# Optimization experiments

Measured on AMD Instinct MI355X. Metric: run time of the kernel, lower is better.

Reference implementation:

```python
import jax, jax.numpy as jnp
import numpy as np

N, D, H, E = 50000, 128, 128, 800000


def setup_inputs() -> dict:
    key = jax.random.key(0)
    ks = jax.random.split(key, 12)
    p = lambda k, shape: jax.random.normal(k, shape, dtype=jnp.float32) * 0.02
    z = lambda n: jnp.zeros((n,), jnp.float32)
    return {
        "x1": jax.random.normal(ks[0], (N, D), dtype=jnp.float32),
        "edge_index1": jax.random.randint(ks[1], (2, E), 0, N, dtype=jnp.int32),
        "x2": jax.random.normal(ks[2], (N, D), dtype=jnp.float32),
        "edge_index2": jax.random.randint(ks[3], (2, E), 0, N, dtype=jnp.int32),
        "enc_w1": p(ks[4], (D, H)), "enc_b1": z(H),
        "enc_w2": p(ks[5], (H, H)), "enc_b2": z(H),
        "conv1_w": p(ks[6], (H, H)), "conv1_b": z(H),
        "conv2_w": p(ks[7], (H, H)), "conv2_b": z(H),
        "sim_w1": p(ks[8], (4 * H, H)), "sim_b1": z(H),
        "sim_w2": p(ks[9], (H, 1)), "sim_b2": z(1),
    }


def reference(x1, edge_index1, x2, edge_index2,
              enc_w1, enc_b1, enc_w2, enc_b2,
              conv1_w, conv1_b, conv2_w, conv2_b,
              sim_w1, sim_b1, sim_w2, sim_b2):
    def gcn(x, ei, W, b):
        row, col = ei[0], ei[1]            # [E], [E]
        h = x @ W + b                      # [N, H]
        n = x.shape[0]
        deg = jax.ops.segment_sum(jnp.ones(row.shape[0], h.dtype), row, num_segments=n)
        dis = jnp.where(deg > 0, deg ** -0.5, 0.0)   # deg^-0.5, inf -> 0
        norm = dis[row] * dis[col]         # [E]
        msg = h[col] * norm[:, None]       # gather + per-edge scale, [E, H]
        return jax.ops.segment_sum(msg, row, num_segments=n)  # scatter-add

    def embed(x, ei):
        h = jax.nn.relu(x @ enc_w1 + enc_b1) @ enc_w2 + enc_b2  # encoder MLP
        h = jax.nn.relu(gcn(h, ei, conv1_w, conv1_b))
        h = jax.nn.relu(gcn(h, ei, conv2_w, conv2_b))
        return h.mean(axis=0)              # mean pooling -> [H]

    g1 = embed(x1, edge_index1)
    g2 = embed(x2, edge_index2)
    c = jnp.concatenate([g1, g2, jnp.abs(g1 - g2), g1 * g2], axis=-1)  # [4H]
    return jax.nn.relu(c @ sim_w1 + sim_b1) @ sim_w2 + sim_b2          # [1]
```

## Files before the change

### kernel.cpp

```cpp
#include <hip/hip_runtime.h>

#define HD 128

typedef _Float16 f16x8 __attribute__((ext_vector_type(8)));
typedef _Float16 f16x2 __attribute__((ext_vector_type(2)));
typedef float f32x4 __attribute__((ext_vector_type(4)));

__device__ __forceinline__ void role_map(int bi, int S, int k, int& role, int& rid) {
  int q = bi / k, rem = bi - q * k;
  if (rem == 0 && q < S) { role = 1; rid = q; }
  else { role = 0; int na = q + (rem ? 1 : 0); if (na > S) na = S; rid = bi - na; }
}

__global__ void k_wcvt(const float* __restrict__ w0, const float* __restrict__ w1,
                       const float* __restrict__ w2, const float* __restrict__ w3,
                       _Float16* __restrict__ Wf) {
  int m = blockIdx.x >> 3;
  const float* Wg = (m == 0) ? w0 : (m == 1) ? w1 : (m == 2) ? w2 : w3;
  int idx0 = (blockIdx.x & 7) * 2048 + threadIdx.x * 8;
  float4 u0 = *(const float4*)(Wg + idx0);
  float4 u1 = *(const float4*)(Wg + idx0 + 4);
  int k = idx0 >> 7, n0 = idx0 & 127;
  int kc = k >> 5, q2 = (k >> 3) & 3, j = k & 7;
  _Float16* dst = Wf + (size_t)m * 16384;
  float vv[8] = {u0.x, u0.y, u0.z, u0.w, u1.x, u1.y, u1.z, u1.w};
  #pragma unroll
  for (int d = 0; d < 8; ++d) {
    int n = n0 + d;
    dst[(size_t)(((n >> 4) * 4 + kc) * 64 + 16 * q2 + (n & 15)) * 8 + j] = (_Float16)vv[d];
  }
}

__device__ __forceinline__ void deg_core(int rid, int degB,
    const int* __restrict__ ei0, const int* __restrict__ ei1, int E, int N,
    int* __restrict__ deg2, unsigned short* __restrict__ slot) {
  int g = (rid >= degB);
  int cb = rid - g * degB;
  const int* rows = g ? ei1 : ei0;
  int* deg = deg2 + g * N;
  unsigned short* sl = slot + (size_t)g * E;
  int base = (cb * 256 + threadIdx.x) * 4;
  if (base + 3 < E) {
    int4 r = *(const int4*)(rows + base);
    union { unsigned short us[4]; uint2 v; } s;
    s.us[0] = (unsigned short)atomicAdd(&deg[r.x], 1);
    s.us[1] = (unsigned short)atomicAdd(&deg[r.y], 1);
    s.us[2] = (unsigned short)atomicAdd(&deg[r.z], 1);
    s.us[3] = (unsigned short)atomicAdd(&deg[r.w], 1);
    *(uint2*)(sl + base) = s.v;
  } else {
    for (int e = base; e < E; ++e)
      sl[e] = (unsigned short)atomicAdd(&deg[rows[e]], 1);
  }
}

__device__ __forceinline__ void fill_core(int rid, int fillB,
    const int* __restrict__ ei0, const int* __restrict__ ei1, int E, int N,
    const int* __restrict__ offs, const int* __restrict__ partials,
    const unsigned short* __restrict__ slot, unsigned short* __restrict__ csr_col) {
  int g = (rid >= fillB);
  int cb = rid - g * fillB;
  const int* eg = (g ? ei1 : ei0);
  const int* ob = offs + g * N;
  const unsigned short* sl = slot + (size_t)g * E;
  int gN = g * N;
  int base = (cb * 256 + threadIdx.x) * 4;
  if (base + 3 < E) {
    int4 r = *(const int4*)(eg + base);
    int4 c = *(const int4*)(eg + E + base);
    uint2 sv = *(const uint2*)(sl + base);
    csr_col[ob[r.x] + partials[(gN + r.x) >> 8] + (sv.x & 0xffff)] = (unsigned short)c.x;
    csr_col[ob[r.y] + partials[(gN + r.y) >> 8] + (sv.x >> 16)]    = (unsigned short)c.y;
    csr_col[ob[r.z] + partials[(gN + r.z) >> 8] + (sv.y & 0xffff)] = (unsigned short)c.z;
    csr_col[ob[r.w] + partials[(gN + r.w) >> 8] + (sv.y >> 16)]    = (unsigned short)c.w;
  } else {
    for (int e = base; e < E; ++e)
      csr_col[ob[eg[e]] + partials[(gN + eg[e]) >> 8] + sl[e]] = (unsigned short)eg[E + e];
  }
}

__device__ __forceinline__ void gemm_core(_Float16* lds, int bi,
    const _Float16* __restrict__ Ab, const _Float16* __restrict__ Wf,
    const float* __restrict__ bias, const float* __restrict__ scale,
    _Float16* __restrict__ C, int Ntot) {
  const int tid = threadIdx.x;
  #pragma unroll
  for (int i = 0; i < 8; ++i)
    *(float4*)&lds[tid * 8 + i * 2048] = *(const float4*)&Wf[tid * 8 + i * 2048];
  __syncthreads();

  const int lane = tid & 63, wave = tid >> 6;
  const int n16 = lane & 15, q = lane >> 4;
  const int rowbase = bi * 128 + wave * 32;

  int arow[2];
  #pragma unroll
  for (int t = 0; t < 2; ++t) {
    int r = rowbase + 16 * t + n16;
    arow[t] = (r < Ntot) ? r : (Ntot - 1);
  }
  f32x4 acc[2][8];
  #pragma unroll
  for (int t = 0; t < 2; ++t)
    #pragma unroll
    for (int nt = 0; nt < 8; ++nt) acc[t][nt] = (f32x4){0.f, 0.f, 0.f, 0.f};

  #pragma unroll
  for (int kc = 0; kc < 4; ++kc) {
    f16x8 a[2];
    #pragma unroll
    for (int t = 0; t < 2; ++t)
      a[t] = *(const f16x8*)(Ab + (size_t)arow[t] * HD + kc * 32 + q * 8);
    #pragma unroll
    for (int nt = 0; nt < 8; ++nt) {
      f16x8 b = *(const f16x8*)&lds[(size_t)((nt * 4 + kc) * 64 + lane) * 8];
      #pragma unroll
      for (int t = 0; t < 2; ++t)
        acc[t][nt] = __builtin_amdgcn_mfma_f32_16x16x32_f16(a[t], b, acc[t][nt], 0, 0, 0);
    }
  }
  float bv[8];
  #pragma unroll
  for (int nt = 0; nt < 8; ++nt) bv[nt] = bias[nt * 16 + n16];
  #pragma unroll
  for (int t = 0; t < 2; ++t) {
    #pragma unroll
    for (int r = 0; r < 4; ++r) {
      int row = rowbase + 16 * t + 4 * q + r;
      if (row < Ntot) {
        float s = scale[row];
        #pragma unroll
        for (int nt = 0; nt < 8; ++nt) {
          float v = (acc[t][nt][r] + bv[nt]) * s;
          C[(size_t)row * HD + nt * 16 + n16] = (_Float16)v;
        }
      }
    }
  }
}

__device__ __forceinline__ void chain_core(_Float16* act, int bi,
    const float* __restrict__ x0, const float* __restrict__ x1,
    const _Float16* __restrict__ Wf0, const _Float16* __restrict__ Wf1,
    const float* __restrict__ b1, const float* __restrict__ b2,
    _Float16* __restrict__ H, int N, int Ntot) {
  const int tid = threadIdx.x;
  const int lane = tid & 63, wave = tid >> 6;
  const int n16 = lane & 15, q = lane >> 4;
  const int rowbase = bi * 128 + wave * 32;
  _Float16* wact = act + wave * 4352;

  int arow[2];
  #pragma unroll
  for (int t = 0; t < 2; ++t) {
    int r = rowbase + 16 * t + n16;
    arow[t] = (r < Ntot) ? r : (Ntot - 1);
  }
  f32x4 acc[2][8];
  #pragma unroll
  for (int t = 0; t < 2; ++t)
    #pragma unroll
    for (int nt = 0; nt < 8; ++nt) acc[t][nt] = (f32x4){0.f, 0.f, 0.f, 0.f};

  #pragma unroll
  for (int kc = 0; kc < 4; ++kc) {
    f16x8 a[2];
    #pragma unroll
    for (int t = 0; t < 2; ++t) {
      int r = arow[t];
      const float* src = (r < N) ? (x0 + (size_t)r * HD) : (x1 + (size_t)(r - N) * HD);
      float4 u0 = *(const float4*)(src + kc * 32 + q * 8);
      float4 u1 = *(const float4*)(src + kc * 32 + q * 8 + 4);
      union { _Float16 h[8]; f16x8 v; } tmp;
      tmp.h[0] = (_Float16)u0.x; tmp.h[1] = (_Float16)u0.y;
      tmp.h[2] = (_Float16)u0.z; tmp.h[3] = (_Float16)u0.w;
      tmp.h[4] = (_Float16)u1.x; tmp.h[5] = (_Float16)u1.y;
      tmp.h[6] = (_Float16)u1.z; tmp.h[7] = (_Float16)u1.w;
      a[t] = tmp.v;
    }
    #pragma unroll
    for (int nt = 0; nt < 8; ++nt) {
      f16x8 b = *(const f16x8*)&Wf0[(size_t)((nt * 4 + kc) * 64 + lane) * 8];
      #pragma unroll
      for (int t = 0; t < 2; ++t)
        acc[t][nt] = __builtin_amdgcn_mfma_f32_16x16x32_f16(a[t], b, acc[t][nt], 0, 0, 0);
    }
  }
  {
    float bv[8];
    #pragma unroll
    for (int nt = 0; nt < 8; ++nt) bv[nt] = b1[nt * 16 + n16];
    #pragma unroll
    for (int t = 0; t < 2; ++t)
      #pragma unroll
      for (int r = 0; r < 4; ++r)
        #pragma unroll
        for (int nt = 0; nt < 8; ++nt)
          wact[(16 * t + 4 * q + r) * 136 + nt * 16 + n16] =
              (_Float16)fmaxf(acc[t][nt][r] + bv[nt], 0.f);
  }

  #pragma unroll
  for (int t = 0; t < 2; ++t)
    #pragma unroll
    for (int nt = 0; nt < 8; ++nt) acc[t][nt] = (f32x4){0.f, 0.f, 0.f, 0.f};
  #pragma unroll
  for (int kc = 0; kc < 4; ++kc) {
    f16x8 a[2];
    #pragma unroll
    for (int t = 0; t < 2; ++t)
      a[t] = *(const f16x8*)&wact[(16 * t + n16) * 136 + kc * 32 + q * 8];
    #pragma unroll
    for (int nt = 0; nt < 8; ++nt) {
      f16x8 b = *(const f16x8*)&Wf1[(size_t)((nt * 4 + kc) * 64 + lane) * 8];
      #pragma unroll
      for (int t = 0; t < 2; ++t)
        acc[t][nt] = __builtin_amdgcn_mfma_f32_16x16x32_f16(a[t], b, acc[t][nt], 0, 0, 0);
    }
  }
  {
    float bv[8];
    #pragma unroll
    for (int nt = 0; nt < 8; ++nt) bv[nt] = b2[nt * 16 + n16];
    #pragma unroll
    for (int t = 0; t < 2; ++t)
      #pragma unroll
      for (int r = 0; r < 4; ++r) {
        int row = rowbase + 16 * t + 4 * q + r;
        if (row < Ntot)
          #pragma unroll
          for (int nt = 0; nt < 8; ++nt)
            H[(size_t)row * HD + nt * 16 + n16] = (_Float16)(acc[t][nt][r] + bv[nt]);
      }
  }
}

template<bool POOL>
__device__ __forceinline__ void agg_core(float* red, int rid,
    const _Float16* __restrict__ T, const int* __restrict__ offs,
    const int* __restrict__ partials, const unsigned short* __restrict__ csr_col,
    const float* __restrict__ dis, _Float16* __restrict__ out,
    float* __restrict__ poolrep, int N, int Ntot, int Etot) {
  const int lane = threadIdx.x & 63;
  const int wave = threadIdx.x >> 6;
  const int gw = rid * 4 + wave;
  const int sub = lane >> 4, c16 = lane & 15;

  f16x2 hacc[4];
  #pragma unroll
  for (int j = 0; j < 4; ++j) hacc[j] = (f16x2){(_Float16)0.f, (_Float16)0.f};

  const int beg = offs[gw] + partials[gw >> 8];
  const int end = (gw + 1 == Ntot) ? Etot : (offs[gw + 1] + partials[(gw + 1) >> 8]);
  const uint4* Tg = (const uint4*)(T + (size_t)(gw >= N ? N : 0) * HD);
  for (int e = beg; e < end; e += 16) {
    uint4 v[4];
    #pragma unroll
    for (int gp = 0; gp < 4; ++gp) {
      v[gp] = make_uint4(0, 0, 0, 0);
      if (e + 4 * gp < end) {
        int eg = e + 4 * gp + sub;
        bool valid = (eg < end);
        int ce = valid ? eg : (end - 1);
        int col = csr_col[ce];
        uint4 tv = Tg[(size_t)col * 16 + c16];
        if (valid) v[gp] = tv;
      }
    }
    #pragma unroll
    for (int gp = 0; gp < 4; ++gp) {
      union { uint4 u; f16x2 h[4]; } w;
      w.u = v[gp];
      hacc[0] += w.h[0];
      hacc[1] += w.h[1];
      hacc[2] += w.h[2];
      hacc[3] += w.h[3];
    }
  }

  float ax[8];
  #pragma unroll
  for (int j = 0; j < 4; ++j) {
    ax[2 * j]     = (float)hacc[j][0];
    ax[2 * j + 1] = (float)hacc[j][1];
  }
  #pragma unroll
  for (int j = 0; j < 8; ++j) {
    ax[j] += __shfl_xor(ax[j], 32, 64);
    ax[j] += __shfl_xor(ax[j], 16, 64);
  }
  float dr = dis[gw];
  #pragma unroll
  for (int j = 0; j < 8; ++j) ax[j] = fmaxf(ax[j] * dr, 0.f);

  if (!POOL) {
    if (sub == 0) {
      union { uint4 u; _Float16 h[8]; } o;
      #pragma unroll
      for (int j = 0; j < 8; ++j) o.h[j] = (_Float16)ax[j];
      ((uint4*)out)[(size_t)gw * 16 + c16] = o.u;
    }
  } else {
    if (sub == 0) {
      *(float4*)&red[wave * 128 + c16 * 8]     = make_float4(ax[0], ax[1], ax[2], ax[3]);
      *(float4*)&red[wave * 128 + c16 * 8 + 4] = make_float4(ax[4], ax[5], ax[6], ax[7]);
    }
    __syncthreads();
    int t = threadIdx.x;
    if (t < 128) {
      float s = red[t] + red[128 + t] + red[256 + t] + red[384 + t];
      int g = (rid * 4 >= N) ? 1 : 0;
      atomicAdd(&poolrep[(size_t)((rid & 15) * 2 + g) * 128 + t], s);
    }
  }
}

__global__ __launch_bounds__(256, 4) void k_d1(
    const float* __restrict__ x0, const float* __restrict__ x1,
    const _Float16* __restrict__ Wf, const float* __restrict__ b1,
    const float* __restrict__ b2, _Float16* __restrict__ H,
    const int* __restrict__ ei0, const int* __restrict__ ei1, int E, int N, int Ntot,
    int* __restrict__ deg2, unsigned short* __restrict__ slot, int G, int A, int degB) {
  __shared__ _Float16 act[4 * 4352];
  int role, rid;
  role_map(blockIdx.x, G, (A + G) / G, role, rid);
  if (role == 1)
    chain_core(act, rid, x0, x1, Wf, Wf + 16384, b1, b2, H, N, Ntot);
  else
    deg_core(rid, degB, ei0, ei1, E, N, deg2, slot);
}

__global__ __launch_bounds__(256, 2) void k_scan(
    const int* __restrict__ deg2, int* __restrict__ offs, int* __restrict__ partials,
    float* __restrict__ dis, int Ntot, int scanB, int* __restrict__ ctr) {
  __shared__ int s[512];
  __shared__ int lastFlag;
  int rid = blockIdx.x, t = threadIdx.x;
  int i = rid * 256 + t;
  int v = (i < Ntot) ? deg2[i] : 0;
  s[t] = v;
  __syncthreads();
  #pragma unroll
  for (int off = 1; off < 256; off <<= 1) {
    int x = (t >= off) ? s[t - off] : 0;
    __syncthreads();
    s[t] += x;
    __syncthreads();
  }
  if (i < Ntot) {
    offs[i] = s[t] - v;
    dis[i] = (v > 0) ? (1.0f / sqrtf((float)v)) : 0.0f;
  }
  if (t == 255) partials[rid] = s[255];
  __syncthreads();
  if (t == 0) {
    __threadfence();
    lastFlag = (atomicAdd(ctr, 1) == scanB - 1);
  }
  __syncthreads();
  if (lastFlag) {
    __threadfence();
    volatile int* vp = partials;
    int P = scanB;
    int v0 = (t < P) ? vp[t] : 0;
    int v1 = (t + 256 < P) ? vp[t + 256] : 0;
    __syncthreads();
    s[t] = v0;
    s[t + 256] = v1;
    __syncthreads();
    #pragma unroll
    for (int off = 1; off < 256; off <<= 1) {
      int x0 = (t >= off) ? s[t - off] : 0;
      int x1 = (t >= off) ? s[256 + t - off] : 0;
      __syncthreads();
      s[t] += x0;
      s[256 + t] += x1;
      __syncthreads();
    }
    int tot0 = s[255];
    if (t < P) partials[t] = s[t] - v0;
    if (t + 256 < P) partials[t + 256] = s[256 + t] + tot0 - v1;
  }
}

__global__ __launch_bounds__(256, 4) void k_conv1_fill(
    const _Float16* __restrict__ Ain, const _Float16* __restrict__ Wf,
    const float* __restrict__ bias, const float* __restrict__ dis,
    _Float16* __restrict__ Cout, int Ntot, int G,
    const int* __restrict__ ei0, const int* __restrict__ ei1, int E, int N,
    const int* __restrict__ offs, const int* __restrict__ partials,
    const unsigned short* __restrict__ slot, unsigned short* __restrict__ csr_col,
    int fillB) {
  __shared__ _Float16 lds[16384];
  int role, rid;
  role_map(blockIdx.x, G, 3, role, rid);
  if (role == 1)
    gemm_core(lds, rid, Ain, Wf, bias, dis, Cout, Ntot);
  else
    fill_core(rid, fillB, ei0, ei1, E, N, offs, partials, slot, csr_col);
}

__global__ __launch_bounds__(256) void k_agg(
    const _Float16* __restrict__ T, const int* __restrict__ offs,
    const int* __restrict__ partials, const unsigned short* __restrict__ csr_col,
    const float* __restrict__ dis, _Float16* __restrict__ out, int N, int Ntot, int Etot) {
  agg_core<false>(nullptr, blockIdx.x, T, offs, partials, csr_col, dis,
                  out, nullptr, N, Ntot, Etot);
}

__global__ __launch_bounds__(256, 4) void k_gemm(
    const _Float16* __restrict__ Ain, const _Float16* __restrict__ Wf,
    const float* __restrict__ bias, const float* __restrict__ dis,
    _Float16* __restrict__ Cout, int Ntot) {
  __shared__ _Float16 lds[16384];
  gemm_core(lds, blockIdx.x, Ain, Wf, bias, dis, Cout, Ntot);
}

__global__ __launch_bounds__(256) void k_agg_pool(
    const _Float16* __restrict__ T, const int* __restrict__ offs,
    const int* __restrict__ partials, const unsigned short* __restrict__ csr_col,
    const float* __restrict__ dis, float* __restrict__ poolrep,
    int N, int Ntot, int Etot) {
  __shared__ float red[512];
  agg_core<true>(red, blockIdx.x, T, offs, partials, csr_col, dis,
                 nullptr, poolrep, N, Ntot, Etot);
}

__global__ void k_final(const float* __restrict__ poolrep,
                        const float* __restrict__ W1, const float* __restrict__ b1,
                        const float* __restrict__ W2, const float* __restrict__ b2,
                        float* __restrict__ out, float invN) {
  __shared__ float cs[512];
  __shared__ float red[2];
  int t = threadIdx.x;
  float g1 = 0.f, g2 = 0.f;
  #pragma unroll
  for (int r = 0; r < 16; ++r) {
    g1 += poolrep[r * 256 + t];
    g2 += poolrep[r * 256 + 128 + t];
  }
  g1 *= invN;
  g2 *= invN;
  cs[t] = g1;
  cs[128 + t] = g2;
  cs[256 + t] = fabsf(g1 - g2);
  cs[384 + t] = g1 * g2;
  __syncthreads();
  float acc = b1[t];
  #pragma unroll 8
  for (int i = 0; i < 512; ++i) acc = fmaf(cs[i], W1[(size_t)i * HD + t], acc);
  float h = fmaxf(acc, 0.f);
  float v = h * W2[t];
  #pragma unroll
  for (int off = 32; off > 0; off >>= 1) v += __shfl_down(v, off, 64);
  if ((t & 63) == 0) red[t >> 6] = v;
  __syncthreads();
  if (t == 0) out[0] = red[0] + red[1] + b2[0];
}

extern "C" void kernel_launch(void* const* d_in, const int* in_sizes, int n_in,
                              void* d_out, int out_size, void* d_ws, size_t ws_size,
                              hipStream_t stream) {
  const float* x1     = (const float*)d_in[0];
  const int*   ei1    = (const int*)d_in[1];
  const float* x2     = (const float*)d_in[2];
  const int*   ei2    = (const int*)d_in[3];
  const float* W_in[4] = {(const float*)d_in[4], (const float*)d_in[6],
                          (const float*)d_in[8], (const float*)d_in[10]};
  const float* B_in[4] = {(const float*)d_in[5], (const float*)d_in[7],
                          (const float*)d_in[9], (const float*)d_in[11]};
  const float* sim_w1 = (const float*)d_in[12];
  const float* sim_b1 = (const float*)d_in[13];
  const float* sim_w2 = (const float*)d_in[14];
  const float* sim_b2 = (const float*)d_in[15];

  const int N = in_sizes[0] / HD;
  const int E = in_sizes[1] / 2;
  const int Ntot = 2 * N;

  _Float16* sp = (_Float16*)d_ws;
  _Float16* bufA = sp; sp += (size_t)Ntot * HD;
  _Float16* bufB = sp; sp += (size_t)Ntot * HD;
  _Float16* bufC = sp; sp += (size_t)Ntot * HD;
  _Float16* WfB  = sp; sp += 4 * 16384;
  float* fp = (float*)sp;
  float* dis     = fp; fp += Ntot;
  float* poolrep = fp; fp += 16 * 256;
  int* ip = (int*)fp;
  int* ctrs     = ip; ip += 8;
  int* deg2     = ip; ip += Ntot;
  int* offs     = ip; ip += Ntot;
  int* partials = ip; ip += 512;
  ip = (int*)(((uintptr_t)ip + 15) & ~(uintptr_t)15);
  unsigned short* slot = (unsigned short*)ip;
  unsigned short* csr_col = slot + 2 * (size_t)E;

  const int G1    = (Ntot + 127) / 128;
  const int scanB = (Ntot + 255) / 256;
  const int aggB  = Ntot / 4;
  const int degB  = ((E + 3) / 4 + 255) / 256;
  const int fillB = degB;

  hipMemsetAsync(poolrep, 0, (16 * 256 + 8 + Ntot) * sizeof(float), stream);

  k_wcvt<<<32, 256, 0, stream>>>(W_in[0], W_in[1], W_in[2], W_in[3], WfB);

  k_d1<<<2 * degB + G1, 256, 0, stream>>>(
      x1, x2, WfB, B_in[0], B_in[1], bufA, ei1, ei2, E, N, Ntot,
      deg2, slot, G1, 2 * degB, degB);

  k_scan<<<scanB, 256, 0, stream>>>(deg2, offs, partials, dis, Ntot, scanB, ctrs);

  k_conv1_fill<<<2 * fillB + G1, 256, 0, stream>>>(
      bufA, WfB + 2 * 16384, B_in[2], dis, bufB, Ntot, G1,
      ei1, ei2, E, N, offs, partials, slot, csr_col, fillB);

  k_agg<<<aggB, 256, 0, stream>>>(bufB, offs, partials, csr_col, dis, bufC, N, Ntot, 2 * E);

  k_gemm<<<G1, 256, 0, stream>>>(bufC, WfB + 3 * 16384, B_in[3], dis, bufA, Ntot);

  k_agg_pool<<<aggB, 256, 0, stream>>>(bufA, offs, partials, csr_col, dis, poolrep,
                                       N, Ntot, 2 * E);

  k_final<<<1, 128, 0, stream>>>(poolrep, sim_w1, sim_b1, sim_w2, sim_b2,
                                 (float*)d_out, 1.0f / (float)N);
}
```

Measured before the change: 404.4 us.

## Store GCN messages in scaled FP8 and compute CSR slots with fill-time atomics

The per-node transformed features used in the gather-aggregate kernels are now stored as FP8 with a fixed 8192 scale, halving the bytes gathered per edge, and accumulated in fp32 after unpacking. The degree pass no longer records per-edge slot indices; instead the CSR fill pass claims positions with a second atomic counter array. This cuts gather bandwidth and the slot array traffic, but adds extra atomics in the fill phase and loses precision through FP8 quantization with a fixed scale that may underflow or saturate depending on value range.

```diff
diff --git a/kernel.cpp b/kernel.cpp
--- a/kernel.cpp
+++ b/kernel.cpp
@@ -1,10 +1,16 @@
 #include <hip/hip_runtime.h>
 
 #define HD 128
+#define FP8_SCALE 8192.0f
+#define FP8_INV   (1.0f / 8192.0f)
 
 typedef _Float16 f16x8 __attribute__((ext_vector_type(8)));
-typedef _Float16 f16x2 __attribute__((ext_vector_type(2)));
 typedef float f32x4 __attribute__((ext_vector_type(4)));
+typedef float f32x2 __attribute__((ext_vector_type(2)));
+
+static __device__ __forceinline__ unsigned char f32_to_fp8(float v) {
+  return (unsigned char)(__builtin_amdgcn_cvt_pk_fp8_f32(v, v, 0, false) & 0xff);
+}
 
 __device__ __forceinline__ void role_map(int bi, int S, int k, int& role, int& rid) {
   int q = bi / k, rem = bi - q * k;
@@ -33,56 +39,58 @@
 
 __device__ __forceinline__ void deg_core(int rid, int degB,
     const int* __restrict__ ei0, const int* __restrict__ ei1, int E, int N,
-    int* __restrict__ deg2, unsigned short* __restrict__ slot) {
+    int* __restrict__ deg2) {
   int g = (rid >= degB);
   int cb = rid - g * degB;
   const int* rows = g ? ei1 : ei0;
   int* deg = deg2 + g * N;
-  unsigned short* sl = slot + (size_t)g * E;
   int base = (cb * 256 + threadIdx.x) * 4;
   if (base + 3 < E) {
     int4 r = *(const int4*)(rows + base);
-    union { unsigned short us[4]; uint2 v; } s;
-    s.us[0] = (unsigned short)atomicAdd(&deg[r.x], 1);
-    s.us[1] = (unsigned short)atomicAdd(&deg[r.y], 1);
-    s.us[2] = (unsigned short)atomicAdd(&deg[r.z], 1);
-    s.us[3] = (unsigned short)atomicAdd(&deg[r.w], 1);
-    *(uint2*)(sl + base) = s.v;
+    atomicAdd(&deg[r.x], 1);
+    atomicAdd(&deg[r.y], 1);
+    atomicAdd(&deg[r.z], 1);
+    atomicAdd(&deg[r.w], 1);
   } else {
-    for (int e = base; e < E; ++e)
-      sl[e] = (unsigned short)atomicAdd(&deg[rows[e]], 1);
+    for (int e = base; e < E; ++e) atomicAdd(&deg[rows[e]], 1);
   }
 }
 
 __device__ __forceinline__ void fill_core(int rid, int fillB,
     const int* __restrict__ ei0, const int* __restrict__ ei1, int E, int N,
     const int* __restrict__ offs, const int* __restrict__ partials,
-    const unsigned short* __restrict__ slot, unsigned short* __restrict__ csr_col) {
+    int* __restrict__ cnt, unsigned short* __restrict__ csr_col) {
   int g = (rid >= fillB);
   int cb = rid - g * fillB;
   const int* eg = (g ? ei1 : ei0);
   const int* ob = offs + g * N;
-  const unsigned short* sl = slot + (size_t)g * E;
   int gN = g * N;
   int base = (cb * 256 + threadIdx.x) * 4;
   if (base + 3 < E) {
     int4 r = *(const int4*)(eg + base);
     int4 c = *(const int4*)(eg + E + base);
-    uint2 sv = *(const uint2*)(sl + base);
-    csr_col[ob[r.x] + partials[(gN + r.x) >> 8] + (sv.x & 0xffff)] = (unsigned short)c.x;
-    csr_col[ob[r.y] + partials[(gN + r.y) >> 8] + (sv.x >> 16)]    = (unsigned short)c.y;
-    csr_col[ob[r.z] + partials[(gN + r.z) >> 8] + (sv.y & 0xffff)] = (unsigned short)c.z;
-    csr_col[ob[r.w] + partials[(gN + r.w) >> 8] + (sv.y >> 16)]    = (unsigned short)c.w;
+    int p0 = ob[r.x] + partials[(gN + r.x) >> 8] + atomicAdd(&cnt[gN + r.x], 1);
+    int p1 = ob[r.y] + partials[(gN + r.y) >> 8] + atomicAdd(&cnt[gN + r.y], 1);
+    int p2 = ob[r.z] + partials[(gN + r.z) >> 8] + atomicAdd(&cnt[gN + r.z], 1);
+    int p3 = ob[r.w] + partials[(gN + r.w) >> 8] + atomicAdd(&cnt[gN + r.w], 1);
+    csr_col[p0] = (unsigned short)c.x;
+    csr_col[p1] = (unsigned short)c.y;
+    csr_col[p2] = (unsigned short)c.z;
+    csr_col[p3] = (unsigned short)c.w;
   } else {
-    for (int e = base; e < E; ++e)
-      csr_col[ob[eg[e]] + partials[(gN + eg[e]) >> 8] + sl[e]] = (unsigned short)eg[E + e];
-  }
-}
-
+    for (int e = base; e < E; ++e) {
+      int r = eg[e];
+      int p = ob[r] + partials[(gN + r) >> 8] + atomicAdd(&cnt[gN + r], 1);
+      csr_col[p] = (unsigned short)eg[E + e];
+    }
+  }
+}
+
+template<bool FP8>
 __device__ __forceinline__ void gemm_core(_Float16* lds, int bi,
     const _Float16* __restrict__ Ab, const _Float16* __restrict__ Wf,
     const float* __restrict__ bias, const float* __restrict__ scale,
-    _Float16* __restrict__ C, int Ntot) {
+    void* __restrict__ Cv, int Ntot) {
   const int tid = threadIdx.x;
   #pragma unroll
   for (int i = 0; i < 8; ++i)
@@ -132,7 +140,11 @@
         #pragma unroll
         for (int nt = 0; nt < 8; ++nt) {
           float v = (acc[t][nt][r] + bv[nt]) * s;
-          C[(size_t)row * HD + nt * 16 + n16] = (_Float16)v;
+          if (FP8)
+            ((unsigned char*)Cv)[(size_t)row * HD + nt * 16 + n16] =
+                f32_to_fp8(v * FP8_SCALE);
+          else
+            ((_Float16*)Cv)[(size_t)row * HD + nt * 16 + n16] = (_Float16)v;
         }
       }
     }
@@ -237,7 +249,7 @@
 
 template<bool POOL>
 __device__ __forceinline__ void agg_core(float* red, int rid,
-    const _Float16* __restrict__ T, const int* __restrict__ offs,
+    const unsigned char* __restrict__ T8, const int* __restrict__ offs,
     const int* __restrict__ partials, const unsigned short* __restrict__ csr_col,
     const float* __restrict__ dis, _Float16* __restrict__ out,
     float* __restrict__ poolrep, int N, int Ntot, int Etot) {
@@ -246,50 +258,46 @@
   const int gw = rid * 4 + wave;
   const int sub = lane >> 4, c16 = lane & 15;
 
-  f16x2 hacc[4];
-  #pragma unroll
-  for (int j = 0; j < 4; ++j) hacc[j] = (f16x2){(_Float16)0.f, (_Float16)0.f};
+  float ax[8];
+  #pragma unroll
+  for (int j = 0; j < 8; ++j) ax[j] = 0.f;
 
   const int beg = offs[gw] + partials[gw >> 8];
   const int end = (gw + 1 == Ntot) ? Etot : (offs[gw + 1] + partials[(gw + 1) >> 8]);
-  const uint4* Tg = (const uint4*)(T + (size_t)(gw >= N ? N : 0) * HD);
+  const uint2* Tg = (const uint2*)(T8 + (size_t)(gw >= N ? N : 0) * HD);
   for (int e = beg; e < end; e += 16) {
-    uint4 v[4];
+    uint2 v[4];
     #pragma unroll
     for (int gp = 0; gp < 4; ++gp) {
-      v[gp] = make_uint4(0, 0, 0, 0);
+      v[gp] = make_uint2(0, 0);
       if (e + 4 * gp < end) {
         int eg = e + 4 * gp + sub;
         bool valid = (eg < end);
         int ce = valid ? eg : (end - 1);
         int col = csr_col[ce];
-        uint4 tv = Tg[(size_t)col * 16 + c16];
+        uint2 tv = Tg[(size_t)col * 16 + c16];
         if (valid) v[gp] = tv;
       }
     }
     #pragma unroll
     for (int gp = 0; gp < 4; ++gp) {
-      union { uint4 u; f16x2 h[4]; } w;
-      w.u = v[gp];
-      hacc[0] += w.h[0];
-      hacc[1] += w.h[1];
-      hacc[2] += w.h[2];
-      hacc[3] += w.h[3];
-    }
-  }
-
-  float ax[8];
-  #pragma unroll
-  for (int j = 0; j < 4; ++j) {
-    ax[2 * j]     = (float)hacc[j][0];
-    ax[2 * j + 1] = (float)hacc[j][1];
-  }
+      f32x2 p0 = __builtin_amdgcn_cvt_pk_f32_fp8((int)v[gp].x, false);
+      f32x2 p1 = __builtin_amdgcn_cvt_pk_f32_fp8((int)v[gp].x, true);
+      f32x2 p2 = __builtin_amdgcn_cvt_pk_f32_fp8((int)v[gp].y, false);
+      f32x2 p3 = __builtin_amdgcn_cvt_pk_f32_fp8((int)v[gp].y, true);
+      ax[0] += p0.x; ax[1] += p0.y;
+      ax[2] += p1.x; ax[3] += p1.y;
+      ax[4] += p2.x; ax[5] += p2.y;
+      ax[6] += p3.x; ax[7] += p3.y;
+    }
+  }
+
   #pragma unroll
   for (int j = 0; j < 8; ++j) {
     ax[j] += __shfl_xor(ax[j], 32, 64);
     ax[j] += __shfl_xor(ax[j], 16, 64);
   }
-  float dr = dis[gw];
+  float dr = dis[gw] * FP8_INV;
   #pragma unroll
   for (int j = 0; j < 8; ++j) ax[j] = fmaxf(ax[j] * dr, 0.f);
 
@@ -320,14 +328,14 @@
     const _Float16* __restrict__ Wf, const float* __restrict__ b1,
     const float* __restrict__ b2, _Float16* __restrict__ H,
     const int* __restrict__ ei0, const int* __restrict__ ei1, int E, int N, int Ntot,
-    int* __restrict__ deg2, unsigned short* __restrict__ slot, int G, int A, int degB) {
+    int* __restrict__ deg2, int G, int A, int degB) {
   __shared__ _Float16 act[4 * 4352];
   int role, rid;
   role_map(blockIdx.x, G, (A + G) / G, role, rid);
   if (role == 1)
     chain_core(act, rid, x0, x1, Wf, Wf + 16384, b1, b2, H, N, Ntot);
   else
-    deg_core(rid, degB, ei0, ei1, E, N, deg2, slot);
+    deg_core(rid, degB, ei0, ei1, E, N, deg2);
 }
 
 __global__ __launch_bounds__(256, 2) void k_scan(
@@ -386,43 +394,42 @@
 __global__ __launch_bounds__(256, 4) void k_conv1_fill(
     const _Float16* __restrict__ Ain, const _Float16* __restrict__ Wf,
     const float* __restrict__ bias, const float* __restrict__ dis,
-    _Float16* __restrict__ Cout, int Ntot, int G,
+    unsigned char* __restrict__ Cout, int Ntot, int G,
     const int* __restrict__ ei0, const int* __restrict__ ei1, int E, int N,
     const int* __restrict__ offs, const int* __restrict__ partials,
-    const unsigned short* __restrict__ slot, unsigned short* __restrict__ csr_col,
-    int fillB) {
+    int* __restrict__ cnt, unsigned short* __restrict__ csr_col, int fillB) {
   __shared__ _Float16 lds[16384];
   int role, rid;
   role_map(blockIdx.x, G, 3, role, rid);
   if (role == 1)
-    gemm_core(lds, rid, Ain, Wf, bias, dis, Cout, Ntot);
+    gemm_core<true>(lds, rid, Ain, Wf, bias, dis, Cout, Ntot);
   else
-    fill_core(rid, fillB, ei0, ei1, E, N, offs, partials, slot, csr_col);
+    fill_core(rid, fillB, ei0, ei1, E, N, offs, partials, cnt, csr_col);
 }
 
 __global__ __launch_bounds__(256) void k_agg(
-    const _Float16* __restrict__ T, const int* __restrict__ offs,
+    const unsigned char* __restrict__ T8, const int* __restrict__ offs,
     const int* __restrict__ partials, const unsigned short* __restrict__ csr_col,
     const float* __restrict__ dis, _Float16* __restrict__ out, int N, int Ntot, int Etot) {
-  agg_core<false>(nullptr, blockIdx.x, T, offs, partials, csr_col, dis,
+  agg_core<false>(nullptr, blockIdx.x, T8, offs, partials, csr_col, dis,
                   out, nullptr, N, Ntot, Etot);
 }
 
 __global__ __launch_bounds__(256, 4) void k_gemm(
     const _Float16* __restrict__ Ain, const _Float16* __restrict__ Wf,
     const float* __restrict__ bias, const float* __restrict__ dis,
-    _Float16* __restrict__ Cout, int Ntot) {
+    unsigned char* __restrict__ Cout, int Ntot) {
   __shared__ _Float16 lds[16384];
-  gemm_core(lds, blockIdx.x, Ain, Wf, bias, dis, Cout, Ntot);
+  gemm_core<true>(lds, blockIdx.x, Ain, Wf, bias, dis, Cout, Ntot);
 }
 
 __global__ __launch_bounds__(256) void k_agg_pool(
-    const _Float16* __restrict__ T, const int* __restrict__ offs,
+    const unsigned char* __restrict__ T8, const int* __restrict__ offs,
     const int* __restrict__ partials, const unsigned short* __restrict__ csr_col,
     const float* __restrict__ dis, float* __restrict__ poolrep,
     int N, int Ntot, int Etot) {
   __shared__ float red[512];
-  agg_core<true>(red, blockIdx.x, T, offs, partials, csr_col, dis,
+  agg_core<true>(red, blockIdx.x, T8, offs, partials, csr_col, dis,
                  nullptr, poolrep, N, Ntot, Etot);
 }
 
@@ -480,8 +487,9 @@
 
   _Float16* sp = (_Float16*)d_ws;
   _Float16* bufA = sp; sp += (size_t)Ntot * HD;
-  _Float16* bufB = sp; sp += (size_t)Ntot * HD;
   _Float16* bufC = sp; sp += (size_t)Ntot * HD;
+  unsigned char* bufT8 = (unsigned char*)sp;
+  sp += (size_t)Ntot * HD / 2;
   _Float16* WfB  = sp; sp += 4 * 16384;
   float* fp = (float*)sp;
   float* dis     = fp; fp += Ntot;
@@ -489,11 +497,11 @@
   int* ip = (int*)fp;
   int* ctrs     = ip; ip += 8;
   int* deg2     = ip; ip += Ntot;
+  int* cnt      = ip; ip += Ntot;
   int* offs     = ip; ip += Ntot;
   int* partials = ip; ip += 512;
   ip = (int*)(((uintptr_t)ip + 15) & ~(uintptr_t)15);
-  unsigned short* slot = (unsigned short*)ip;
-  unsigned short* csr_col = slot + 2 * (size_t)E;
+  unsigned short* csr_col = (unsigned short*)ip;
 
   const int G1    = (Ntot + 127) / 128;
   const int scanB = (Ntot + 255) / 256;
@@ -501,25 +509,25 @@
   const int degB  = ((E + 3) / 4 + 255) / 256;
   const int fillB = degB;
 
-  hipMemsetAsync(poolrep, 0, (16 * 256 + 8 + Ntot) * sizeof(float), stream);
+  hipMemsetAsync(poolrep, 0, (16 * 256 + 8 + 2 * Ntot) * sizeof(float), stream);
 
   k_wcvt<<<32, 256, 0, stream>>>(W_in[0], W_in[1], W_in[2], W_in[3], WfB);
 
   k_d1<<<2 * degB + G1, 256, 0, stream>>>(
       x1, x2, WfB, B_in[0], B_in[1], bufA, ei1, ei2, E, N, Ntot,
-      deg2, slot, G1, 2 * degB, degB);
+      deg2, G1, 2 * degB, degB);
 
   k_scan<<<scanB, 256, 0, stream>>>(deg2, offs, partials, dis, Ntot, scanB, ctrs);
 
   k_conv1_fill<<<2 * fillB + G1, 256, 0, stream>>>(
-      bufA, WfB + 2 * 16384, B_in[2], dis, bufB, Ntot, G1,
-      ei1, ei2, E, N, offs, partials, slot, csr_col, fillB);
-
-  k_agg<<<aggB, 256, 0, stream>>>(bufB, offs, partials, csr_col, dis, bufC, N, Ntot, 2 * E);
-
-  k_gemm<<<G1, 256, 0, stream>>>(bufC, WfB + 3 * 16384, B_in[3], dis, bufA, Ntot);
-
-  k_agg_pool<<<aggB, 256, 0, stream>>>(bufA, offs, partials, csr_col, dis, poolrep,
+      bufA, WfB + 2 * 16384, B_in[2], dis, bufT8, Ntot, G1,
+      ei1, ei2, E, N, offs, partials, cnt, csr_col, fillB);
+
+  k_agg<<<aggB, 256, 0, stream>>>(bufT8, offs, partials, csr_col, dis, bufC, N, Ntot, 2 * E);
+
+  k_gemm<<<G1, 256, 0, stream>>>(bufC, WfB + 3 * 16384, B_in[3], dis, bufT8, Ntot);
+
+  k_agg_pool<<<aggB, 256, 0, stream>>>(bufT8, offs, partials, csr_col, dis, poolrep,
                                        N, Ntot, 2 * E);
 
   k_final<<<1, 128, 0, stream>>>(poolrep, sim_w1, sim_b1, sim_w2, sim_b2,
```

Result: slower. 439.0 us (+8.6%).
